# Kernel tuning notes

Measured on AMD Instinct MI355X. Metric: run time of the kernel, lower is better.

The kernel has to match this reference:

```python
import jax, jax.numpy as jnp
import numpy as np

V = 30522   # bert-base-uncased vocab
E = 512     # embed_size
ATT = 512   # attention_dim
ENC = 2048  # encoder_dim
H = 512     # decoder_dim
B = 32
N = 49      # num image features (7x7)
T = 21      # caption length -> 20 decode steps


def setup_inputs() -> dict:
    key = jax.random.key(0)
    ks = jax.random.split(key, 12)
    s = lambda i, shape: jax.random.normal(ks[i], shape, jnp.float32) * 0.02
    features = jax.random.normal(ks[0], (B, N, ENC), jnp.float32)
    captions = jax.random.randint(ks[1], (B, T), 0, V, dtype=jnp.int32)
    return dict(
        features=features, captions=captions,
        emb=s(2, (V, E)),
        W_w=s(3, (ATT, H)), W_b=jnp.zeros((ATT,), jnp.float32),
        U_w=s(4, (ATT, ENC)), U_b=jnp.zeros((ATT,), jnp.float32),
        A_w=s(5, (1, ATT)), A_b=jnp.zeros((1,), jnp.float32),
        init_h_w=s(6, (H, ENC)), init_h_b=jnp.zeros((H,), jnp.float32),
        init_c_w=s(7, (H, ENC)), init_c_b=jnp.zeros((H,), jnp.float32),
        w_ih=s(8, (4 * H, E + ENC)), w_hh=s(9, (4 * H, H)),
        b_ih=jnp.zeros((4 * H,), jnp.float32), b_hh=jnp.zeros((4 * H,), jnp.float32),
        fcn_w=s(10, (V, H)), fcn_b=jnp.zeros((V,), jnp.float32),
    )


def reference(features, captions, emb, W_w, W_b, U_w, U_b, A_w, A_b,
              init_h_w, init_h_b, init_c_w, init_c_b,
              w_ih, w_hh, b_ih, b_hh, fcn_w, fcn_b):
    embeds = emb[captions]                      # [B, T, E]
    mean_f = features.mean(axis=1)              # [B, ENC]
    h0 = mean_f @ init_h_w.T + init_h_b         # [B, H]
    c0 = mean_f @ init_c_w.T + init_c_b
    # U(features) is h-independent: precompute once (same math as per-step in torch)
    u_hs = jnp.einsum('bne,ae->bna', features, U_w) + U_b  # [B, N, ATT]

    def step(carry, x_t):
        h, c = carry
        # Bahdanau attention
        w_ah = h @ W_w.T + W_b                               # [B, ATT]
        scores = jnp.tanh(u_hs + w_ah[:, None, :]) @ A_w[0] + A_b[0]  # [B, N]
        alpha = jax.nn.softmax(scores, axis=1)
        context = jnp.einsum('bn,bne->be', alpha, features)  # [B, ENC]
        # LSTMCell (torch gate order: i, f, g, o)
        lstm_in = jnp.concatenate([x_t, context], axis=1)    # [B, E+ENC]
        gates = lstm_in @ w_ih.T + b_ih + h @ w_hh.T + b_hh  # [B, 4H]
        i, f, g, o = jnp.split(gates, 4, axis=1)
        c2 = jax.nn.sigmoid(f) * c + jax.nn.sigmoid(i) * jnp.tanh(g)
        h2 = jax.nn.sigmoid(o) * jnp.tanh(c2)
        # dropout in eval mode = identity
        out = h2 @ fcn_w.T + fcn_b                           # [B, V]
        return (h2, c2), (out, alpha)

    xs = jnp.swapaxes(embeds[:, :-1], 0, 1)  # [T-1, B, E]
    _, (preds, alphas) = jax.lax.scan(step, (h0, c0), xs)
    return jnp.swapaxes(preds, 0, 1), jnp.swapaxes(alphas, 0, 1)
```

## Files before the change

kernel.cpp:

```cpp
#include <hip/hip_runtime.h>
#include <hip/hip_bf16.h>

#define VCB 30522
#define EMB 512
#define ATTD 512
#define ENC 2048
#define HD 512
#define BB 32
#define NF 49
#define TSTEPS 20
#define EIN 2560
#define KCAT 3072
#define WSTRIDE 3080
#define DTPB 512
#define NBLK 128

typedef __attribute__((ext_vector_type(8))) __bf16 bf16x8;
typedef __attribute__((ext_vector_type(4))) __bf16 bf16x4;
typedef __attribute__((ext_vector_type(4))) float floatx4;
typedef __hip_bfloat16 bf16;

__device__ __forceinline__ float bf2f(bf16 x){ return __bfloat162float(x); }
__device__ __forceinline__ bf16 f2bf(float x){ return __float2bfloat16(x); }
__device__ __forceinline__ float sigm(float x){ return 1.0f/(1.0f+expf(-x)); }
__device__ __forceinline__ float fast_tanh(float x){
    float e2 = __expf(2.0f*x);
    return 1.0f - 2.0f*__builtin_amdgcn_rcpf(e2 + 1.0f);
}

__device__ __forceinline__ unsigned coh_ld(const unsigned* p){
    return __hip_atomic_load(p, __ATOMIC_RELAXED, __HIP_MEMORY_SCOPE_AGENT);
}
__device__ __forceinline__ void coh_st(unsigned* p, unsigned v){
    __hip_atomic_store(p, v, __ATOMIC_RELAXED, __HIP_MEMORY_SCOPE_AGENT);
}
__device__ __forceinline__ unsigned pack2bf(float a, float b){
    unsigned short ua = __builtin_bit_cast(unsigned short, f2bf(a));
    unsigned short ub = __builtin_bit_cast(unsigned short, f2bf(b));
    return (unsigned)ua | ((unsigned)ub << 16);
}

__device__ __forceinline__ void gpost(unsigned* ctr){
    __syncthreads();
    if (threadIdx.x == 0)
        __hip_atomic_fetch_add(ctr, 1u, __ATOMIC_RELAXED, __HIP_MEMORY_SCOPE_AGENT);
}
__device__ __forceinline__ void gwait(const unsigned* ctr, unsigned tgt,
                                      volatile unsigned* sflag){
    float x = 1.0f;
    if (threadIdx.x < 64){
        while (coh_ld(ctr) < tgt){
#pragma unroll
            for (int i = 0; i < 8; ++i)
                x = __builtin_fmaf(x, 1.0000001f, 1e-12f);
        }
        if (threadIdx.x == 0) *sflag = tgt;
    } else {
        while (*sflag < tgt){
#pragma unroll
            for (int i = 0; i < 32; ++i)
                x = __builtin_fmaf(x, 1.0000001f, 1e-12f);
        }
    }
    asm volatile("" :: "v"(x));
    __syncthreads();
}

__device__ __forceinline__ float ld1(const void* base, size_t idx, int f){
    if (f) return ((const float*)base)[idx];
    return bf2f(((const bf16*)base)[idx]);
}
__device__ __forceinline__ bf16x8 ldbf8(const void* base, size_t idx, int f){
    if (f){
        const float* p = (const float*)base + idx;
        float4 a = *(const float4*)p, b = *(const float4*)(p+4);
        bf16x8 r;
        r[0]=(__bf16)a.x; r[1]=(__bf16)a.y; r[2]=(__bf16)a.z; r[3]=(__bf16)a.w;
        r[4]=(__bf16)b.x; r[5]=(__bf16)b.y; r[6]=(__bf16)b.z; r[7]=(__bf16)b.w;
        return r;
    }
    return *(const bf16x8*)((const bf16*)base + idx);
}
__device__ __forceinline__ bf16x8 bf8_of_f32(const float* p){
    float4 a = *(const float4*)p, b = *(const float4*)(p+4);
    bf16x8 r;
    r[0]=(__bf16)a.x; r[1]=(__bf16)a.y; r[2]=(__bf16)a.z; r[3]=(__bf16)a.w;
    r[4]=(__bf16)b.x; r[5]=(__bf16)b.y; r[6]=(__bf16)b.z; r[7]=(__bf16)b.w;
    return r;
}
__device__ __forceinline__ void st1(void* base, size_t idx, float v, int f){
    if (f) ((float*)base)[idx] = v;
    else   ((bf16*)base)[idx] = f2bf(v);
}

#define MFMA16(a,b,c) __builtin_amdgcn_mfma_f32_16x16x32_bf16(a,b,c,0,0,0)

__global__ void k_detect(const void* emb, int* flag, unsigned* bar){
    int tid = threadIdx.x;
    __shared__ int bad;
    if (tid == 0) bad = 0;
    for (int i = tid; i < 1024; i += 256) bar[i] = 0u;
    __syncthreads();
    const unsigned short* u = (const unsigned short*)emb;
    int local = 0;
    for (int i = tid; i < 4096; i += 256){
        int e = (u[i] >> 7) & 0xFF;
        if (e > 140) local = 1;
    }
    if (local) bad = 1;
    __syncthreads();
    if (tid == 0) *flag = bad;
}

__global__ void k_prep_gates(const void* w_ih, const void* w_hh, bf16* __restrict__ wcat,
                             const int* __restrict__ flag){
    int ff = *flag;
    int r = blockIdx.x, tid = threadIdx.x;
    for (int i = tid*8; i < KCAT; i += 2048){
        bf16x8 v;
        if (i + 8 <= EIN){
            v = ldbf8(w_ih, (size_t)r*EIN + i, ff);
        } else if (i >= EIN){
            v = ldbf8(w_hh, (size_t)r*HD + (i - EIN), ff);
        } else {
#pragma unroll
            for (int j = 0; j < 8; ++j){
                int k = i + j;
                v[j] = (__bf16)((k < EIN) ? ld1(w_ih, (size_t)r*EIN + k, ff)
                                          : ld1(w_hh, (size_t)r*HD + (k - EIN), ff));
            }
        }
        *(bf16x8*)(wcat + (size_t)r*KCAT + i) = v;
    }
}
__global__ void k_prep_cvt8(const void* src, bf16* __restrict__ dst, size_t n8,
                            const int* __restrict__ flag){
    int ff = *flag;
    size_t idx = (size_t)blockIdx.x*256 + threadIdx.x;
    size_t stride = (size_t)gridDim.x*256;
    for (size_t i = idx; i < n8; i += stride)
        *(bf16x8*)(dst + i*8) = ldbf8(src, i*8, ff);
}

__global__ void k_mean(const void* feat, float* __restrict__ mean_f,
                       const int* __restrict__ flag){
    int ff = *flag;
    int b = blockIdx.x, tid = threadIdx.x;
    for (int i = 0; i < ENC/256; ++i){
        int e = i*256 + tid;
        size_t base = (size_t)b*NF*ENC + e;
        float s = 0.f;
        for (int n = 0; n < NF; ++n) s += ld1(feat, base + (size_t)n*ENC, ff);
        mean_f[b*ENC + e] = s * (1.0f/49.0f);
    }
}

__global__ void k_init_hc(const float* __restrict__ mean_f,
                          const void* ihw, const void* ihb,
                          const void* icw, const void* icb,
                          float* __restrict__ Hbuf, float* __restrict__ c_f32,
                          const int* __restrict__ flag){
    int ff = *flag;
    int tid = threadIdx.x, wave = tid>>6, lane = tid&63, quad = lane>>4, lq = lane&15;
    int n0 = blockIdx.x*16;
    int ng = n0 + lq;
    const void* w = (ng < HD) ? ihw : icw;
    size_t wrow = (size_t)(ng < HD ? ng : ng - HD)*ENC;
    floatx4 acc[2] = {{0,0,0,0},{0,0,0,0}};
    int kb = wave*512;
    for (int kk = 0; kk < 16; ++kk){
        int k = kb + kk*32 + quad*8;
        bf16x8 bfr = ldbf8(w, wrow + k, ff);
#pragma unroll
        for (int mt = 0; mt < 2; ++mt){
            bf16x8 afr = bf8_of_f32(mean_f + (size_t)(mt*16+lq)*ENC + k);
            acc[mt] = MFMA16(afr, bfr, acc[mt]);
        }
    }
    __shared__ float red[4][2][16][16];
#pragma unroll
    for (int mt = 0; mt < 2; ++mt)
        for (int r = 0; r < 4; ++r)
            red[wave][mt][quad*4+r][lq] = acc[mt][r];
    __syncthreads();
    for (int rep = 0; rep < 2; ++rep){
        int idx = rep*256 + tid;
        int mt = idx>>8, mm = (idx>>4)&15, nn = idx&15;
        float v = red[0][mt][mm][nn]+red[1][mt][mm][nn]+red[2][mt][mm][nn]+red[3][mt][mm][nn];
        int n_g = n0 + nn, b = mt*16 + mm;
        if (n_g < HD) Hbuf[b*HD + n_g]        = v + ld1(ihb, n_g, ff);
        else          c_f32[b*HD + (n_g-HD)]  = v + ld1(icb, n_g - HD, ff);
    }
}

__global__ void k_uhs(const bf16* __restrict__ feat_bf, const void* U_w, const void* U_b,
                      float* __restrict__ u_hs, const int* __restrict__ flag){
    int ff = *flag;
    int tid = threadIdx.x, wave = tid>>6, lane = tid&63, quad = lane>>4, lq = lane&15;
    int m0 = blockIdx.x*16;
    int n0 = blockIdx.y*64 + wave*16;
    size_t arow = (size_t)(m0+lq)*ENC;
    size_t brow = (size_t)(n0+lq)*ENC;
    floatx4 acc = {0,0,0,0};
    for (int kk = 0; kk < ENC/32; ++kk){
        int k = kk*32 + quad*8;
        bf16x8 afr = *(const bf16x8*)(feat_bf + arow + k);
        bf16x8 bfr = ldbf8(U_w,  brow + k, ff);
        acc = MFMA16(afr, bfr, acc);
    }
    float ub = ld1(U_b, n0+lq, ff);
    for (int r = 0; r < 4; ++r){
        int m = m0 + quad*4 + r;
        u_hs[(size_t)m*ATTD + n0 + lq] = acc[r] + ub;
    }
}

__global__ void __launch_bounds__(DTPB) k_decode(
        float* __restrict__ Hbuf, const float* __restrict__ c0_f32,
        const bf16* __restrict__ Ww_bf, const void* __restrict__ W_b,
        const float* __restrict__ u_hs, const void* __restrict__ A_w,
        const void* __restrict__ A_b, const int* __restrict__ captions,
        const void* __restrict__ emb, const bf16* __restrict__ feat_bf,
        bf16* __restrict__ lstm_in, const bf16* __restrict__ wcat,
        const void* __restrict__ b_ih, const void* __restrict__ b_hh,
        bf16* __restrict__ Hall_bf, void* __restrict__ d_out,
        const int* __restrict__ flag, unsigned* __restrict__ bar,
        float* __restrict__ wah_u, float* __restrict__ alpha_u)
{
    const int ff = *flag;
    const int bid = blockIdx.x, tid = threadIdx.x;
    const int wave = tid>>6, lane = tid&63, quad = lane>>4, lq = lane&15;

    __shared__ bf16  wlds[16*WSTRIDE];
    __shared__ float ubuf[4096];
    __shared__ float aw_s[ATTD];
    __shared__ float c_loc[BB*4];
    __shared__ float gbias[16];
    __shared__ unsigned sfW, sfS, sfL, sfH;

    unsigned* lin_u = (unsigned*)lstm_in;
    unsigned* flagW = bar;
    unsigned* flagS = bar + 64;
    unsigned* flagL = bar + 128;
    unsigned* flagH = bar + 192;
    unsigned* wahu_u  = (unsigned*)wah_u;
    unsigned* alphu_u = (unsigned*)alpha_u;

    if (tid == 0){ sfW = 0u; sfS = 0u; sfL = 0u; sfH = 0u; }

    for (int n = 0; n < 16; ++n){
        int g = n>>2, j = n&3;
        const bf16* src = wcat + (size_t)(g*HD + (bid<<2) + j)*KCAT;
        for (int c8 = tid; c8 < KCAT/8; c8 += DTPB)
            *(bf16x8*)(wlds + n*WSTRIDE + c8*8) = *(const bf16x8*)(src + c8*8);
    }
    if (tid < 128){
        int bb = tid&31, j = tid>>5, col = (bid<<2)+j;
        c_loc[bb*4+j] = c0_f32[bb*HD + col];
    }
    if (tid < 64){
        int bb = tid&31, j2 = tid>>5;
        int c0 = (bid<<2) + 2*j2;
        float h0 = Hbuf[bb*HD + c0], h1 = Hbuf[bb*HD + c0 + 1];
        coh_st(lin_u + (size_t)bb*(KCAT/2) + (EIN + c0)/2, pack2bf(h0, h1));
    }
    if (tid < 16){
        int g = tid>>2, j = tid&3, col = (bid<<2)+j;
        gbias[tid] = ld1(b_ih, g*HD+col, ff) + ld1(b_hh, g*HD+col, ff);
    }
    if (bid < BB)
        for (int i = tid; i < ATTD; i += DTPB) aw_s[i] = ld1(A_w, i, ff);
    gpost(flagH);

    float* wah_s   = ubuf + 512;
    float* sc_s    = ubuf + 1024;
    float* alpha_s = ubuf + 1088;
    float (*red)[2][16][16] = (float (*)[2][16][16])ubuf;

    for (int t = 0; t < TSTEPS; ++t){
        if (bid < BB){
            gwait(flagH, 128u*(unsigned)(t+1), &sfH);
            {
                int n0 = bid<<4;
                int kb = wave*64;
                floatx4 acc0 = {0,0,0,0}, acc1 = {0,0,0,0};
                const bf16* brow = Ww_bf + (size_t)(n0+lq)*HD;
                union U8 { unsigned u[4]; bf16x8 v; };
#pragma unroll
                for (int kk = 0; kk < 2; ++kk){
                    int k = kb + kk*32 + quad*8;
                    bf16x8 bfr = *(const bf16x8*)(brow + k);
                    U8 a0, a1;
                    const unsigned* ar0 = lin_u + (size_t)lq*(KCAT/2) + (EIN+k)/2;
                    const unsigned* ar1 = lin_u + (size_t)(16+lq)*(KCAT/2) + (EIN+k)/2;
#pragma unroll
                    for (int q = 0; q < 4; ++q){
                        a0.u[q] = coh_ld(ar0 + q);
                        a1.u[q] = coh_ld(ar1 + q);
                    }
                    acc0 = MFMA16(a0.v, bfr, acc0);
                    acc1 = MFMA16(a1.v, bfr, acc1);
                }
#pragma unroll
                for (int r = 0; r < 4; ++r){
                    red[wave][0][quad*4+r][lq] = acc0[r];
                    red[wave][1][quad*4+r][lq] = acc1[r];
                }
            }
            __syncthreads();
            {
                int b = tid>>4, c = tid&15;
                int mt = b>>4, mm = b&15;
                float s = 0.f;
#pragma unroll
                for (int w8 = 0; w8 < 8; ++w8) s += red[w8][mt][mm][c];
                int col = (bid<<4) + c;
                coh_st(wahu_u + (size_t)b*ATTD + col,
                       __float_as_uint(s + ld1(W_b, col, ff)));
            }
            gpost(flagW);

            gwait(flagW, 32u*(unsigned)(t+1), &sfW);
            const int b = bid;
            wah_s[tid] = __uint_as_float(coh_ld(wahu_u + (size_t)b*ATTD + tid));
            __syncthreads();
            {
                int a0 = lane*8;
                for (int n = wave; n < NF; n += 8){
                    const float* up = u_hs + (size_t)(b*NF + n)*ATTD + a0;
                    float4 u0 = *(const float4*)up;
                    float4 u1 = *(const float4*)(up + 4);
                    float p0 = fast_tanh(u0.x + wah_s[a0+0])*aw_s[a0+0]
                             + fast_tanh(u0.y + wah_s[a0+1])*aw_s[a0+1]
                             + fast_tanh(u0.z + wah_s[a0+2])*aw_s[a0+2]
                             + fast_tanh(u0.w + wah_s[a0+3])*aw_s[a0+3];
                    float p1 = fast_tanh(u1.x + wah_s[a0+4])*aw_s[a0+4]
                             + fast_tanh(u1.y + wah_s[a0+5])*aw_s[a0+5]
                             + fast_tanh(u1.z + wah_s[a0+6])*aw_s[a0+6]
                             + fast_tanh(u1.w + wah_s[a0+7])*aw_s[a0+7];
                    float p = p0 + p1;
                    for (int off = 32; off; off >>= 1) p += __shfl_down(p, off);
                    if (lane == 0) sc_s[n] = p + ld1(A_b, 0, ff);
                }
            }
            __syncthreads();
            if (wave == 0){
                float v = (lane < NF) ? sc_s[lane] : -1e30f;
                float mx = v;
                for (int off = 32; off; off >>= 1) mx = fmaxf(mx, __shfl_down(mx, off));
                mx = __shfl(mx, 0);
                float e = (lane < NF) ? expf(v - mx) : 0.f;
                float s = e;
                for (int off = 32; off; off >>= 1) s += __shfl_down(s, off);
                s = __shfl(s, 0);
                if (lane < NF){
                    float al = e / s;
                    coh_st(alphu_u + b*64 + lane, __float_as_uint(al));
                    st1(d_out, (size_t)BB*TSTEPS*VCB + (size_t)b*(TSTEPS*NF) + t*NF + lane, al, ff);
                }
            }
            gpost(flagS);
        }
        gwait(flagS, 32u*(unsigned)(t+1), &sfS);
        {
            const int b = bid>>2, sl = bid&3;
            if (tid < NF) alpha_s[tid] = __uint_as_float(coh_ld(alphu_u + b*64 + tid));
            __syncthreads();
            if (tid < 256){
                int col = sl*512 + 2*tid;
                const bf16* fb = feat_bf + (size_t)b*NF*ENC + col;
                float a0 = 0.f, a1 = 0.f;
#pragma unroll 7
                for (int n = 0; n < NF; ++n){
                    unsigned fv = *(const unsigned*)(fb + (size_t)n*ENC);
                    float lo = __uint_as_float(fv << 16);
                    float hi = __uint_as_float(fv & 0xffff0000u);
                    float al = alpha_s[n];
                    a0 += al*lo; a1 += al*hi;
                }
                coh_st(lin_u + (size_t)b*(KCAT/2) + (EMB+col)/2, pack2bf(a0, a1));
            } else if (tid >= 448){
                int cap = captions[b*21 + t];
                int col = sl*128 + 2*(tid - 448);
                coh_st(lin_u + (size_t)b*(KCAT/2) + col/2,
                       pack2bf(ld1(emb, (size_t)cap*EMB + col,     ff),
                               ld1(emb, (size_t)cap*EMB + col + 1, ff)));
            }
            gpost(flagL);
        }
        gwait(flagL, 128u*(unsigned)(t+1), &sfL);

        {
            int kb = wave*384;
            floatx4 acc0 = {0,0,0,0}, acc1 = {0,0,0,0};
            const bf16* wrow = wlds + (size_t)lq*WSTRIDE;
            const unsigned* ar0 = lin_u + (size_t)lq*(KCAT/2);
            const unsigned* ar1 = lin_u + (size_t)(16+lq)*(KCAT/2);
            union U8 { unsigned u[4]; bf16x8 v; };
#pragma unroll
            for (int kk = 0; kk < 12; ++kk){
                int kd = (kb + kk*32 + quad*8) >> 1;
                bf16x8 bfr = *(const bf16x8*)(wrow + kb + kk*32 + quad*8);
                U8 a0, a1;
#pragma unroll
                for (int q = 0; q < 4; ++q){
                    a0.u[q] = coh_ld(ar0 + kd + q);
                    a1.u[q] = coh_ld(ar1 + kd + q);
                }
                acc0 = MFMA16(a0.v, bfr, acc0);
                acc1 = MFMA16(a1.v, bfr, acc1);
            }
#pragma unroll
            for (int r = 0; r < 4; ++r){
                red[wave][0][quad*4+r][lq] = acc0[r];
                red[wave][1][quad*4+r][lq] = acc1[r];
            }
        }
        __syncthreads();
        if (tid < 64){
            int bb = tid&31, j2 = tid>>5;
            int mt = bb>>4, mm = bb&15;
            float hn[2];
#pragma unroll
            for (int sub = 0; sub < 2; ++sub){
                int j = 2*j2 + sub;
                float G[4];
#pragma unroll
                for (int g = 0; g < 4; ++g){
                    int n = g*4 + j;
                    float s = 0.f;
#pragma unroll
                    for (int w8 = 0; w8 < 8; ++w8) s += red[w8][mt][mm][n];
                    G[g] = s + gbias[n];
                }
                float c_old = c_loc[bb*4+j];
                float c_new = sigm(G[1])*c_old + sigm(G[0])*tanhf(G[2]);
                float h_new = sigm(G[3])*tanhf(c_new);
                c_loc[bb*4+j] = c_new;
                hn[sub] = h_new;
            }
            int colb = (bid<<2) + 2*j2;
            ((unsigned*)Hall_bf)[((size_t)t*BB*HD + bb*HD + colb) >> 1] = pack2bf(hn[0], hn[1]);
            coh_st(lin_u + (size_t)bb*(KCAT/2) + (EIN + colb)/2, pack2bf(hn[0], hn[1]));
        }
        gpost(flagH);
    }
}

__global__ void __launch_bounds__(256) k_fcn(const bf16* __restrict__ Hall_bf,
                                             const bf16* __restrict__ fcnw_bf,
                                             const void* fcn_b, void* d_out,
                                             const int* __restrict__ flag){
    int ff = *flag;
    int tid = threadIdx.x, wave = tid>>6, lane = tid&63, quad = lane>>4, lq = lane&15;
    int n0 = blockIdx.x*64 + wave*16;
    int v = n0 + lq;
    int vc = (v < VCB) ? v : (VCB-1);
    const bf16* brow = fcnw_bf + (size_t)vc*HD;
    bf16x8 bfr[16];
#pragma unroll
    for (int kk = 0; kk < 16; ++kk) bfr[kk] = *(const bf16x8*)(brow + kk*32 + quad*8);
    float bias = ld1(fcn_b, vc, ff);
    for (int mt = 0; mt < 40; ++mt){
        const bf16* arow = Hall_bf + (size_t)(mt*16 + lq)*HD;
        floatx4 acc = {0,0,0,0};
#pragma unroll
        for (int kk = 0; kk < 16; ++kk){
            bf16x8 afr = *(const bf16x8*)(arow + kk*32 + quad*8);
            acc = MFMA16(afr, bfr[kk], acc);
        }
        if (v < VCB){
#pragma unroll
            for (int r = 0; r < 4; ++r){
                int m = mt*16 + quad*4 + r;
                int b = m & 31, tt = m >> 5;
                st1(d_out, (size_t)b*(TSTEPS*VCB) + (size_t)tt*VCB + v, acc[r] + bias, ff);
            }
        }
    }
}

extern "C" void kernel_launch(void* const* d_in, const int* in_sizes, int n_in,
                              void* d_out, int out_size, void* d_ws, size_t ws_size,
                              hipStream_t stream) {
    const void* feat  = d_in[0];
    const int*  caps  = (const int*)d_in[1];
    const void* emb   = d_in[2];
    const void* W_w   = d_in[3];
    const void* W_b   = d_in[4];
    const void* U_w   = d_in[5];
    const void* U_b   = d_in[6];
    const void* A_w   = d_in[7];
    const void* A_b   = d_in[8];
    const void* ihw   = d_in[9];
    const void* ihb   = d_in[10];
    const void* icw   = d_in[11];
    const void* icb   = d_in[12];
    const void* w_ih  = d_in[13];
    const void* w_hh  = d_in[14];
    const void* b_ih  = d_in[15];
    const void* b_hh  = d_in[16];
    const void* fcn_w = d_in[17];
    const void* fcn_b = d_in[18];

    char* ws = (char*)d_ws;
    size_t off = 0;
    float* u_hs    = (float*)(ws + off); off += (size_t)BB*NF*ATTD*4;
    float* c_f32   = (float*)(ws + off); off += (size_t)BB*HD*4;
    float* mean_f  = (float*)(ws + off); off += (size_t)BB*ENC*4;
    float* Hbuf    = (float*)(ws + off); off += (size_t)(TSTEPS+1)*BB*HD*4;
    bf16*  lstm_in = (bf16*) (ws + off); off += (size_t)BB*KCAT*2;
    bf16*  Hall_bf = (bf16*) (ws + off); off += (size_t)TSTEPS*BB*HD*2;
    bf16*  wcat    = (bf16*) (ws + off); off += (size_t)4*HD*KCAT*2;
    bf16*  fcnw_bf = (bf16*) (ws + off); off += (size_t)VCB*HD*2;
    bf16*  Ww_bf   = (bf16*) (ws + off); off += (size_t)ATTD*HD*2;
    bf16*  feat_bf = (bf16*) (ws + off); off += (size_t)BB*NF*ENC*2;
    float* wah_u   = (float*)(ws + off); off += (size_t)BB*ATTD*4;
    float* alpha_u = (float*)(ws + off); off += (size_t)BB*64*4;
    int*   flag    = (int*)  (ws + off); off += 256;
    unsigned* bar  = (unsigned*)(ws + off); off += 4096;
    if (ws_size < off) return;

    k_detect    <<<1, 256, 0, stream>>>(emb, flag, bar);
    k_prep_gates<<<2048, 256, 0, stream>>>(w_ih, w_hh, wcat, flag);
    k_prep_cvt8 <<<2048, 256, 0, stream>>>(fcn_w, fcnw_bf, (size_t)VCB*HD/8, flag);
    k_prep_cvt8 <<<128, 256, 0, stream>>>(W_w, Ww_bf, (size_t)ATTD*HD/8, flag);
    k_prep_cvt8 <<<1024, 256, 0, stream>>>(feat, feat_bf, (size_t)BB*NF*ENC/8, flag);
    k_mean      <<<BB, 256, 0, stream>>>(feat, mean_f, flag);
    k_init_hc   <<<64, 256, 0, stream>>>(mean_f, ihw, ihb, icw, icb, Hbuf, c_f32, flag);
    k_uhs       <<<dim3(98, 8), 256, 0, stream>>>(feat_bf, U_w, U_b, u_hs, flag);

    {
        void* kargs[20] = {
            (void*)&Hbuf, (void*)&c_f32, (void*)&Ww_bf, (void*)&W_b,
            (void*)&u_hs, (void*)&A_w, (void*)&A_b, (void*)&caps,
            (void*)&emb, (void*)&feat_bf, (void*)&lstm_in, (void*)&wcat,
            (void*)&b_ih, (void*)&b_hh, (void*)&Hall_bf, (void*)&d_out,
            (void*)&flag, (void*)&bar, (void*)&wah_u, (void*)&alpha_u
        };
        hipLaunchCooperativeKernel((void*)k_decode, dim3(NBLK), dim3(DTPB),
                                   kargs, 0, stream);
    }

    k_fcn<<<477, 256, 0, stream>>>(Hall_bf, fcnw_bf, fcn_b, d_out, flag);
}
```

Baseline: 1.451 ms.

## Replace atomic counter barriers with per-block flag slots and drop alpha barrier

Grid barriers switch from atomic fetch-add counters to per-block epoch slots, each written by its own block and polled in parallel by one wave using __all. The softmax/alpha stage is now computed redundantly by all four blocks sharing a batch row, so the global barrier and global buffer used to hand alpha between blocks are gone. This cuts one grid-wide sync per decode step and avoids atomic contention, in exchange for four times the attention-score work.

```diff
diff --git a/kernel.cpp b/kernel.cpp
--- a/kernel.cpp
+++ b/kernel.cpp
@@ -40,21 +40,30 @@
     return (unsigned)ua | ((unsigned)ub << 16);
 }
 
-__device__ __forceinline__ void gpost(unsigned* ctr){
+__device__ __forceinline__ void gpost_slot(unsigned* slot, unsigned ep){
     __syncthreads();
-    if (threadIdx.x == 0)
-        __hip_atomic_fetch_add(ctr, 1u, __ATOMIC_RELAXED, __HIP_MEMORY_SCOPE_AGENT);
-}
-__device__ __forceinline__ void gwait(const unsigned* ctr, unsigned tgt,
-                                      volatile unsigned* sflag){
+    if (threadIdx.x == 0) coh_st(slot, ep);
+}
+__device__ __forceinline__ void gwaitN(const unsigned* slots, int two, unsigned tgt,
+                                       volatile unsigned* sflag){
     float x = 1.0f;
     if (threadIdx.x < 64){
-        while (coh_ld(ctr) < tgt){
+        int l = threadIdx.x;
+        for (;;){
+            unsigned a = coh_ld(slots + l);
+            bool ok;
+            if (two){
+                unsigned b = coh_ld(slots + 64 + l);
+                ok = (a >= tgt) && (b >= tgt);
+            } else {
+                ok = (l < 32) ? (a >= tgt) : true;
+            }
+            if (__all(ok)) break;
 #pragma unroll
             for (int i = 0; i < 8; ++i)
                 x = __builtin_fmaf(x, 1.0000001f, 1e-12f);
         }
-        if (threadIdx.x == 0) *sflag = tgt;
+        if (l == 0) *sflag = tgt;
     } else {
         while (*sflag < tgt){
 #pragma unroll
@@ -225,7 +234,7 @@
         const void* __restrict__ b_ih, const void* __restrict__ b_hh,
         bf16* __restrict__ Hall_bf, void* __restrict__ d_out,
         const int* __restrict__ flag, unsigned* __restrict__ bar,
-        float* __restrict__ wah_u, float* __restrict__ alpha_u)
+        float* __restrict__ wah_u)
 {
     const int ff = *flag;
     const int bid = blockIdx.x, tid = threadIdx.x;
@@ -236,17 +245,15 @@
     __shared__ float aw_s[ATTD];
     __shared__ float c_loc[BB*4];
     __shared__ float gbias[16];
-    __shared__ unsigned sfW, sfS, sfL, sfH;
+    __shared__ unsigned sfW, sfL, sfH;
 
     unsigned* lin_u = (unsigned*)lstm_in;
-    unsigned* flagW = bar;
-    unsigned* flagS = bar + 64;
-    unsigned* flagL = bar + 128;
-    unsigned* flagH = bar + 192;
-    unsigned* wahu_u  = (unsigned*)wah_u;
-    unsigned* alphu_u = (unsigned*)alpha_u;
-
-    if (tid == 0){ sfW = 0u; sfS = 0u; sfL = 0u; sfH = 0u; }
+    unsigned* sH = bar;
+    unsigned* sW = bar + 128;
+    unsigned* sL = bar + 256;
+    unsigned* wahu_u = (unsigned*)wah_u;
+
+    if (tid == 0){ sfW = 0u; sfL = 0u; sfH = 0u; }
 
     for (int n = 0; n < 16; ++n){
         int g = n>>2, j = n&3;
@@ -268,9 +275,8 @@
         int g = tid>>2, j = tid&3, col = (bid<<2)+j;
         gbias[tid] = ld1(b_ih, g*HD+col, ff) + ld1(b_hh, g*HD+col, ff);
     }
-    if (bid < BB)
-        for (int i = tid; i < ATTD; i += DTPB) aw_s[i] = ld1(A_w, i, ff);
-    gpost(flagH);
+    for (int i = tid; i < ATTD; i += DTPB) aw_s[i] = ld1(A_w, i, ff);
+    gpost_slot(sH + bid, 1u);
 
     float* wah_s   = ubuf + 512;
     float* sc_s    = ubuf + 1024;
@@ -279,7 +285,7 @@
 
     for (int t = 0; t < TSTEPS; ++t){
         if (bid < BB){
-            gwait(flagH, 128u*(unsigned)(t+1), &sfH);
+            gwaitN(sH, 1, (unsigned)(t+1), &sfH);
             {
                 int n0 = bid<<4;
                 int kb = wave*64;
@@ -318,11 +324,12 @@
                 coh_st(wahu_u + (size_t)b*ATTD + col,
                        __float_as_uint(s + ld1(W_b, col, ff)));
             }
-            gpost(flagW);
-
-            gwait(flagW, 32u*(unsigned)(t+1), &sfW);
-            const int b = bid;
-            wah_s[tid] = __uint_as_float(coh_ld(wahu_u + (size_t)b*ATTD + tid));
+            gpost_slot(sW + bid, (unsigned)(t+1));
+        }
+        gwaitN(sW, 0, (unsigned)(t+1), &sfW);
+        {
+            const int b = bid>>2, sl = bid&3;
+            wah_s[tid & 511] = __uint_as_float(coh_ld(wahu_u + (size_t)b*ATTD + (tid & 511)));
             __syncthreads();
             {
                 int a0 = lane*8;
@@ -355,16 +362,11 @@
                 s = __shfl(s, 0);
                 if (lane < NF){
                     float al = e / s;
-                    coh_st(alphu_u + b*64 + lane, __float_as_uint(al));
-                    st1(d_out, (size_t)BB*TSTEPS*VCB + (size_t)b*(TSTEPS*NF) + t*NF + lane, al, ff);
-                }
-            }
-            gpost(flagS);
-        }
-        gwait(flagS, 32u*(unsigned)(t+1), &sfS);
-        {
-            const int b = bid>>2, sl = bid&3;
-            if (tid < NF) alpha_s[tid] = __uint_as_float(coh_ld(alphu_u + b*64 + tid));
+                    alpha_s[lane] = al;
+                    if (sl == 0)
+                        st1(d_out, (size_t)BB*TSTEPS*VCB + (size_t)b*(TSTEPS*NF) + t*NF + lane, al, ff);
+                }
+            }
             __syncthreads();
             if (tid < 256){
                 int col = sl*512 + 2*tid;
@@ -386,9 +388,9 @@
                        pack2bf(ld1(emb, (size_t)cap*EMB + col,     ff),
                                ld1(emb, (size_t)cap*EMB + col + 1, ff)));
             }
-            gpost(flagL);
-        }
-        gwait(flagL, 128u*(unsigned)(t+1), &sfL);
+            gpost_slot(sL + bid, (unsigned)(t+1));
+        }
+        gwaitN(sL, 1, (unsigned)(t+1), &sfL);
 
         {
             int kb = wave*384;
@@ -443,7 +445,7 @@
             ((unsigned*)Hall_bf)[((size_t)t*BB*HD + bb*HD + colb) >> 1] = pack2bf(hn[0], hn[1]);
             coh_st(lin_u + (size_t)bb*(KCAT/2) + (EIN + colb)/2, pack2bf(hn[0], hn[1]));
         }
-        gpost(flagH);
+        gpost_slot(sH + bid, (unsigned)(t+2));
     }
 }
 
@@ -516,7 +518,6 @@
     bf16*  Ww_bf   = (bf16*) (ws + off); off += (size_t)ATTD*HD*2;
     bf16*  feat_bf = (bf16*) (ws + off); off += (size_t)BB*NF*ENC*2;
     float* wah_u   = (float*)(ws + off); off += (size_t)BB*ATTD*4;
-    float* alpha_u = (float*)(ws + off); off += (size_t)BB*64*4;
     int*   flag    = (int*)  (ws + off); off += 256;
     unsigned* bar  = (unsigned*)(ws + off); off += 4096;
     if (ws_size < off) return;
@@ -531,12 +532,12 @@
     k_uhs       <<<dim3(98, 8), 256, 0, stream>>>(feat_bf, U_w, U_b, u_hs, flag);
 
     {
-        void* kargs[20] = {
+        void* kargs[19] = {
             (void*)&Hbuf, (void*)&c_f32, (void*)&Ww_bf, (void*)&W_b,
             (void*)&u_hs, (void*)&A_w, (void*)&A_b, (void*)&caps,
             (void*)&emb, (void*)&feat_bf, (void*)&lstm_in, (void*)&wcat,
             (void*)&b_ih, (void*)&b_hh, (void*)&Hall_bf, (void*)&d_out,
-            (void*)&flag, (void*)&bar, (void*)&wah_u, (void*)&alpha_u
+            (void*)&flag, (void*)&bar, (void*)&wah_u
         };
         hipLaunchCooperativeKernel((void*)k_decode, dim3(NBLK), dim3(DTPB),
                                    kargs, 0, stream);
```

Result: faster. 1.422 ms (-2.0%).
